# Kernel tuning notes

Measured on AMD Instinct MI355X. Metric: run time of the kernel, lower is better.

Reference implementation:

```python
import jax, jax.numpy as jnp
import numpy as np


def _conv(x, k):
    # x: (B,H,W,Cin), k: (kh,kw,Cin,Cout), SAME padding, stride 1
    return jax.lax.conv_general_dilated(
        x, k, window_strides=(1, 1), padding='SAME',
        dimension_numbers=('NHWC', 'HWIO', 'NHWC'))


def _hard_sigmoid(x):
    # Keras ConvLSTM2D default recurrent_activation='hard_sigmoid'
    return jnp.clip(0.2 * x + 0.5, 0.0, 1.0)


def _convlstm_layer(x_seq, k, rk, b):
    # x_seq: (B,T,H,W,Cin); gates packed i,f,c,o along channel axis (Keras order)
    B, T, H, W, _ = x_seq.shape
    F = rk.shape[2]
    h0 = jnp.zeros((B, H, W, F), x_seq.dtype)
    c0 = jnp.zeros((B, H, W, F), x_seq.dtype)

    def step(carry, xt):
        h, c = carry
        z = _conv(xt, k) + _conv(h, rk) + b
        i, f, g, o = jnp.split(z, 4, axis=-1)
        c_new = _hard_sigmoid(f) * c + _hard_sigmoid(i) * jnp.tanh(g)
        h_new = _hard_sigmoid(o) * jnp.tanh(c_new)
        return (h_new, c_new), h_new

    (h, c), ys = jax.lax.scan(step, (h0, c0), jnp.moveaxis(x_seq, 1, 0))
    return jnp.moveaxis(ys, 0, 1), h, c  # outputs (B,T,H,W,F), final h, c


def setup_inputs() -> dict:
    key = jax.random.key(0)
    ks = jax.random.split(key, 6)
    s = 0.05
    return {
        'x': jax.random.normal(ks[0], (8, 10, 64, 64, 1), jnp.float32),
        'k0': jax.random.normal(ks[1], (3, 3, 1, 256), jnp.float32) * s,
        'rk0': jax.random.normal(ks[2], (3, 3, 64, 256), jnp.float32) * s,
        'b0': jnp.zeros((256,), jnp.float32),
        'k1': jax.random.normal(ks[3], (3, 3, 64, 256), jnp.float32) * s,
        'rk1': jax.random.normal(ks[4], (3, 3, 64, 256), jnp.float32) * s,
        'b1': jnp.zeros((256,), jnp.float32),
    }


def reference(x, k0, rk0, b0, k1, rk1, b1):
    # layer 0
    seq0, h0, c0 = _convlstm_layer(x, k0, rk0, b0)
    # layer 1 consumes layer-0 sequence
    _, h1, c1 = _convlstm_layer(seq0, k1, rk1, b1)
    # states list [[h0,c0],[h1,c1]] -> stacked (layers=2, 2, B, H, W, F)
    return jnp.stack([jnp.stack([h0, c0]), jnp.stack([h1, c1])])
```

## Files before the change

### kernel.cpp

```cpp
#include <hip/hip_runtime.h>
#include <hip/hip_bf16.h>

typedef unsigned short u16;
typedef __attribute__((ext_vector_type(8))) short short8;
typedef __attribute__((ext_vector_type(4))) float f32x4;

#define T_STEPS 10
#define NB 8
#define HH 64
#define WW 64
#define FF 64
#define NGATE 256
#define HP 66
#define PIX (NB*HH*WW)

__device__ __forceinline__ u16 f2bf(float f) {
    unsigned u = __float_as_uint(f);
    u += 0x7FFF + ((u >> 16) & 1);
    return (u16)(u >> 16);
}
__device__ __forceinline__ float hsig(float x) {
    return fminf(fmaxf(0.2f * x + 0.5f, 0.0f), 1.0f);
}
__device__ __forceinline__ float ftanh(float x) {
    float e = __expf(2.0f * x);
    return 1.0f - 2.0f / (e + 1.0f);
}
__device__ __forceinline__ void gll16(const void* g, void* l) {
    __builtin_amdgcn_global_load_lds(
        (const __attribute__((address_space(1))) unsigned*)g,
        (__attribute__((address_space(3))) unsigned*)l, 16, 0, 0);
}

__global__ void wtrans_kernel(const float* __restrict__ W0,
                              const float* __restrict__ W1,
                              u16* __restrict__ BS, int K) {
    int total = (K >> 6) << 14;
    for (int o = blockIdx.x * blockDim.x + threadIdx.x; o < total;
         o += gridDim.x * blockDim.x) {
        int e = o & 7, lane = (o >> 3) & 63, g = (o >> 9) & 3;
        int ks = (o >> 11) & 1, fq = (o >> 12) & 3, kc = o >> 14;
        int quad = lane >> 4, l15 = lane & 15;
        int n = g * 64 + fq * 16 + l15;
        int k = kc * 64 + ks * 32 + quad * 8 + e;
        float v = (k < 576) ? W0[k * NGATE + n] : W1[(k - 576) * NGATE + n];
        BS[o] = f2bf(v);
    }
}

__global__ __launch_bounds__(256, 3)
void fused_step_kernel(const u16* __restrict__ h0_prev, u16* __restrict__ h0_new,
                       const u16* __restrict__ h1_prev, u16* __restrict__ h1_new,
                       const u16* __restrict__ B0S, const u16* __restrict__ B1S,
                       const float* __restrict__ x, const float* __restrict__ k0w,
                       const float* __restrict__ b0, const float* __restrict__ b1,
                       float* __restrict__ c0, float* __restrict__ c1,
                       float* __restrict__ oh0, float* __restrict__ oc0,
                       float* __restrict__ oh1, float* __restrict__ oc1,
                       int u) {
    int blk = blockIdx.x;
    int b = blk & 7;
    int k = blk >> 3;
    int role = ((k >> 5) & 1) ^ 1;
    int y = (k & 31) | ((k >> 6) << 5);
    int pxb = b * 64 + y;
    if (role == 0 && u >= T_STEPS) return;
    if (role == 1 && u == 0) return;

    __shared__ __align__(16) u16 sA[6 * 528 * 8];
    __shared__ float xs[3][WW + 2];

    int tid = threadIdx.x;
    int lane = tid & 63, fq = tid >> 6;
    int quad = lane >> 4, l15 = lane & 15;

    const u16* BS = role ? B1S : B0S;
    int nch = role ? 18 : 9;

    if (role == 0 && tid < 3 * (WW + 2)) {
        int dyi = tid / (WW + 2), xx = tid - dyi * (WW + 2);
        int yy = y + dyi - 1, col = xx - 1;
        float v = 0.0f;
        if (yy >= 0 && yy < HH && col >= 0 && col < WW)
            v = x[(((size_t)b * T_STEPS + u) * HH + yy) * WW + col];
        xs[dyi][xx] = v;
    }

    {
        int nst = role ? 6 * 528 : 3 * 528;
        for (int i = tid; i < nst; i += 256) {
            int srcsel = i >= 3 * 528;
            int q = srcsel ? i - 3 * 528 : i;
            int r = q / 528;
            int qr = q - r * 528;
            int p = qr >> 3;
            int cb = (qr & 7) ^ (p & 7);
            const u16* src = srcsel ? h1_prev : h0_prev;
            gll16(src + (((size_t)(b * HP + y + r)) * HP + p) * FF + cb * 8,
                  &sA[(size_t)i * 8]);
        }
    }
    asm volatile("s_waitcnt vmcnt(0) lgkmcnt(0)\n\ts_barrier" ::: "memory");

    f32x4 acc[4][4];
#pragma unroll
    for (int mt = 0; mt < 4; ++mt)
#pragma unroll
        for (int g = 0; g < 4; ++g)
            acc[mt][g] = (f32x4){0.f, 0.f, 0.f, 0.f};

    const u16* bbase = BS + (fq << 12) + lane * 8;
    short8 bA[8], bB[8];

#pragma unroll
    for (int j = 0; j < 8; ++j)
        bA[j] = *(const short8*)(bbase + ((j >> 2) << 11) + ((j & 3) << 9));

    int dx = 0, srb = 0;

#define KBODY(BC, BN, kcur)                                                   \
    {                                                                         \
        int kn = (kcur) + 1 < nch ? (kcur) + 1 : (kcur);                      \
        const u16* bpn = bbase + ((size_t)kn << 14);                          \
        _Pragma("unroll")                                                     \
        for (int j = 0; j < 8; ++j)                                           \
            BN[j] = *(const short8*)(bpn + ((j >> 2) << 11) + ((j & 3) << 9)); \
        int cc = l15 + dx, sw = cc & 7;                                       \
        const u16* ar = sA + srb + cc * 64;                                   \
        _Pragma("unroll")                                                     \
        for (int ks = 0; ks < 2; ++ks) {                                      \
            short8 aF[4];                                                     \
            int so = (((ks << 2) | quad) ^ sw) << 3;                          \
            _Pragma("unroll")                                                 \
            for (int mt = 0; mt < 4; ++mt)                                    \
                aF[mt] = *(const short8*)(ar + so + mt * 1024);               \
            _Pragma("unroll")                                                 \
            for (int mt = 0; mt < 4; ++mt)                                    \
                _Pragma("unroll")                                             \
                for (int g = 0; g < 4; ++g)                                   \
                    acc[mt][g] = __builtin_amdgcn_mfma_f32_16x16x32_bf16(     \
                        aF[mt], BC[ks * 4 + g], acc[mt][g], 0, 0, 0);         \
        }                                                                     \
        ++dx; if (dx == 3) { dx = 0; srb += 4224; }                           \
    }

    int kc = 0;
    for (; kc + 1 < nch; kc += 2) {
        KBODY(bA, bB, kc);
        KBODY(bB, bA, kc + 1);
    }
    if (kc < nch) KBODY(bA, bB, kc);
#undef KBODY

    const float* bias = role ? b1 : b0;
    float* cbuf = role ? c1 : c0;
    u16* hout = role ? h1_new : h0_new;
    int wo = role ? (u == T_STEPS) : (u == T_STEPS - 1);
    float* outh = role ? oh1 : oh0;
    float* outc = role ? oc1 : oc0;

    int f = fq * 16 + l15;
    float bi = bias[f], bff = bias[64 + f], bg = bias[128 + f], bo = bias[192 + f];
    float wk[4][9];
    if (role == 0) {
#pragma unroll
        for (int g = 0; g < 4; ++g)
#pragma unroll
            for (int tau = 0; tau < 9; ++tau)
                wk[g][tau] = k0w[tau * NGATE + g * 64 + f];
    }
#pragma unroll
    for (int mt = 0; mt < 4; ++mt) {
#pragma unroll
        for (int r = 0; r < 4; ++r) {
            int xcol = mt * 16 + quad * 4 + r;
            size_t p = (size_t)pxb * 64 + xcol;
            float zi = acc[mt][0][r] + bi;
            float zf = acc[mt][1][r] + bff;
            float zg = acc[mt][2][r] + bg;
            float zo = acc[mt][3][r] + bo;
            if (role == 0) {
#pragma unroll
                for (int tau = 0; tau < 9; ++tau) {
                    float xv = xs[tau / 3][xcol + tau % 3];
                    zi += xv * wk[0][tau];
                    zf += xv * wk[1][tau];
                    zg += xv * wk[2][tau];
                    zo += xv * wk[3][tau];
                }
            }
            float cold = cbuf[p * FF + f];
            float cn = hsig(zf) * cold + hsig(zi) * ftanh(zg);
            float hn = hsig(zo) * ftanh(cn);
            cbuf[p * FF + f] = cn;
            hout[(((size_t)(b * HP + y + 1)) * HP + (xcol + 1)) * FF + f] = f2bf(hn);
            if (wo) { outh[p * FF + f] = hn; outc[p * FF + f] = cn; }
        }
    }
}

extern "C" void kernel_launch(void* const* d_in, const int* in_sizes, int n_in,
                              void* d_out, int out_size, void* d_ws, size_t ws_size,
                              hipStream_t stream) {
    const float* x   = (const float*)d_in[0];
    const float* k0  = (const float*)d_in[1];
    const float* rk0 = (const float*)d_in[2];
    const float* b0  = (const float*)d_in[3];
    const float* k1  = (const float*)d_in[4];
    const float* rk1 = (const float*)d_in[5];
    const float* b1  = (const float*)d_in[6];
    float* out = (float*)d_out;

    char* ws = (char*)d_ws;
    const size_t HPAD_BYTES = (size_t)NB * HP * HP * FF * 2;
    const size_t C_BYTES    = (size_t)PIX * FF * 4;

    u16* h0p[2]; u16* h1p[2];
    h0p[0] = (u16*)(ws);
    h0p[1] = (u16*)(ws + HPAD_BYTES);
    h1p[0] = (u16*)(ws + 2 * HPAD_BYTES);
    h1p[1] = (u16*)(ws + 3 * HPAD_BYTES);
    float* c0 = (float*)(ws + 4 * HPAD_BYTES);
    float* c1 = (float*)(ws + 4 * HPAD_BYTES + C_BYTES);
    u16* B0S  = (u16*)(ws + 4 * HPAD_BYTES + 2 * C_BYTES);
    u16* B1S  = (u16*)(ws + 4 * HPAD_BYTES + 2 * C_BYTES + (size_t)9 * 16384 * 2);

    hipMemsetAsync(ws, 0, 4 * HPAD_BYTES + 2 * C_BYTES, stream);

    wtrans_kernel<<<512, 256, 0, stream>>>(rk0, rk0, B0S, 576);
    wtrans_kernel<<<512, 256, 0, stream>>>(k1, rk1, B1S, 1152);

    float* oh0 = out;
    float* oc0 = out + (size_t)PIX * FF;
    float* oh1 = out + 2 * (size_t)PIX * FF;
    float* oc1 = out + 3 * (size_t)PIX * FF;

    for (int u = 0; u <= T_STEPS; ++u) {
        const u16* h0_prev = h0p[(u + 1) & 1];
        u16*       h0_new  = h0p[u & 1];
        const u16* h1_prev = h1p[u & 1];
        u16*       h1_new  = h1p[(u + 1) & 1];
        fused_step_kernel<<<1024, 256, 0, stream>>>(
            h0_prev, h0_new, h1_prev, h1_new, B0S, B1S,
            x, k0, b0, b1, c0, c1, oh0, oc0, oh1, oc1, u);
    }
}
```

Baseline: 503.7 us.

## Merge layer-0 and layer-1 work into one block sharing staged h0 rows

Before, each time step launched 1024 blocks, split into separate layer-0 and layer-1 roles, and each role staged its own copy of the h0_prev halo rows into LDS. Now each of 512 blocks stages h0_prev (and h1_prev) once, then runs the layer-0 GEMM and epilogue followed by the layer-1 GEMM and epilogue in sequence. This removes the duplicated h0 staging and halves block-launch overhead. In exchange, per-block serial work grows and parallelism halves, which may leave the GPU underfilled given 3 blocks per CU.

```diff
diff --git a/kernel.cpp b/kernel.cpp
--- a/kernel.cpp
+++ b/kernel.cpp
@@ -48,76 +48,16 @@
     }
 }
 
-__global__ __launch_bounds__(256, 3)
-void fused_step_kernel(const u16* __restrict__ h0_prev, u16* __restrict__ h0_new,
-                       const u16* __restrict__ h1_prev, u16* __restrict__ h1_new,
-                       const u16* __restrict__ B0S, const u16* __restrict__ B1S,
-                       const float* __restrict__ x, const float* __restrict__ k0w,
-                       const float* __restrict__ b0, const float* __restrict__ b1,
-                       float* __restrict__ c0, float* __restrict__ c1,
-                       float* __restrict__ oh0, float* __restrict__ oc0,
-                       float* __restrict__ oh1, float* __restrict__ oc1,
-                       int u) {
-    int blk = blockIdx.x;
-    int b = blk & 7;
-    int k = blk >> 3;
-    int role = ((k >> 5) & 1) ^ 1;
-    int y = (k & 31) | ((k >> 6) << 5);
-    int pxb = b * 64 + y;
-    if (role == 0 && u >= T_STEPS) return;
-    if (role == 1 && u == 0) return;
-
-    __shared__ __align__(16) u16 sA[6 * 528 * 8];
-    __shared__ float xs[3][WW + 2];
-
-    int tid = threadIdx.x;
-    int lane = tid & 63, fq = tid >> 6;
-    int quad = lane >> 4, l15 = lane & 15;
-
-    const u16* BS = role ? B1S : B0S;
-    int nch = role ? 18 : 9;
-
-    if (role == 0 && tid < 3 * (WW + 2)) {
-        int dyi = tid / (WW + 2), xx = tid - dyi * (WW + 2);
-        int yy = y + dyi - 1, col = xx - 1;
-        float v = 0.0f;
-        if (yy >= 0 && yy < HH && col >= 0 && col < WW)
-            v = x[(((size_t)b * T_STEPS + u) * HH + yy) * WW + col];
-        xs[dyi][xx] = v;
-    }
-
-    {
-        int nst = role ? 6 * 528 : 3 * 528;
-        for (int i = tid; i < nst; i += 256) {
-            int srcsel = i >= 3 * 528;
-            int q = srcsel ? i - 3 * 528 : i;
-            int r = q / 528;
-            int qr = q - r * 528;
-            int p = qr >> 3;
-            int cb = (qr & 7) ^ (p & 7);
-            const u16* src = srcsel ? h1_prev : h0_prev;
-            gll16(src + (((size_t)(b * HP + y + r)) * HP + p) * FF + cb * 8,
-                  &sA[(size_t)i * 8]);
-        }
-    }
-    asm volatile("s_waitcnt vmcnt(0) lgkmcnt(0)\n\ts_barrier" ::: "memory");
-
-    f32x4 acc[4][4];
-#pragma unroll
-    for (int mt = 0; mt < 4; ++mt)
-#pragma unroll
-        for (int g = 0; g < 4; ++g)
-            acc[mt][g] = (f32x4){0.f, 0.f, 0.f, 0.f};
-
+__device__ __forceinline__ void kphase(f32x4 (&acc)[4][4],
+                                       const u16* __restrict__ BS, int nch,
+                                       const u16* __restrict__ sA,
+                                       int lane, int fq, int quad, int l15) {
     const u16* bbase = BS + (fq << 12) + lane * 8;
     short8 bA[8], bB[8];
-
 #pragma unroll
     for (int j = 0; j < 8; ++j)
         bA[j] = *(const short8*)(bbase + ((j >> 2) << 11) + ((j & 3) << 9));
-
     int dx = 0, srb = 0;
-
 #define KBODY(BC, BN, kcur)                                                   \
     {                                                                         \
         int kn = (kcur) + 1 < nch ? (kcur) + 1 : (kcur);                      \
@@ -143,7 +83,6 @@
         }                                                                     \
         ++dx; if (dx == 3) { dx = 0; srb += 4224; }                           \
     }
-
     int kc = 0;
     for (; kc + 1 < nch; kc += 2) {
         KBODY(bA, bB, kc);
@@ -151,18 +90,22 @@
     }
     if (kc < nch) KBODY(bA, bB, kc);
 #undef KBODY
-
-    const float* bias = role ? b1 : b0;
-    float* cbuf = role ? c1 : c0;
-    u16* hout = role ? h1_new : h0_new;
-    int wo = role ? (u == T_STEPS) : (u == T_STEPS - 1);
-    float* outh = role ? oh1 : oh0;
-    float* outc = role ? oc1 : oc0;
-
+}
+
+__device__ __forceinline__ void epilogue(const f32x4 (&acc)[4][4],
+                                         const float* __restrict__ bias,
+                                         float* __restrict__ cbuf,
+                                         u16* __restrict__ hout,
+                                         float* __restrict__ outh,
+                                         float* __restrict__ outc, int wo,
+                                         int withx, const float (*xs)[WW + 2],
+                                         const float* __restrict__ k0w,
+                                         int b, int y, int pxb,
+                                         int fq, int quad, int l15) {
     int f = fq * 16 + l15;
     float bi = bias[f], bff = bias[64 + f], bg = bias[128 + f], bo = bias[192 + f];
     float wk[4][9];
-    if (role == 0) {
+    if (withx) {
 #pragma unroll
         for (int g = 0; g < 4; ++g)
 #pragma unroll
@@ -179,7 +122,7 @@
             float zf = acc[mt][1][r] + bff;
             float zg = acc[mt][2][r] + bg;
             float zo = acc[mt][3][r] + bo;
-            if (role == 0) {
+            if (withx) {
 #pragma unroll
                 for (int tau = 0; tau < 9; ++tau) {
                     float xv = xs[tau / 3][xcol + tau % 3];
@@ -199,6 +142,80 @@
     }
 }
 
+__global__ __launch_bounds__(256, 3)
+void fused_step_kernel(const u16* __restrict__ h0_prev, u16* __restrict__ h0_new,
+                       const u16* __restrict__ h1_prev, u16* __restrict__ h1_new,
+                       const u16* __restrict__ B0S, const u16* __restrict__ B1S,
+                       const float* __restrict__ x, const float* __restrict__ k0w,
+                       const float* __restrict__ b0, const float* __restrict__ b1,
+                       float* __restrict__ c0, float* __restrict__ c1,
+                       float* __restrict__ oh0, float* __restrict__ oc0,
+                       float* __restrict__ oh1, float* __restrict__ oc1,
+                       int u) {
+    int blk = blockIdx.x;
+    int b = blk & 7;
+    int y = blk >> 3;
+    int pxb = b * 64 + y;
+    int do0 = (u < T_STEPS);
+    int do1 = (u > 0);
+
+    __shared__ __align__(16) u16 sA[6 * 528 * 8];
+    __shared__ float xs[3][WW + 2];
+
+    int tid = threadIdx.x;
+    int lane = tid & 63, fq = tid >> 6;
+    int quad = lane >> 4, l15 = lane & 15;
+
+    if (do0 && tid < 3 * (WW + 2)) {
+        int dyi = tid / (WW + 2), xx = tid - dyi * (WW + 2);
+        int yy = y + dyi - 1, col = xx - 1;
+        float v = 0.0f;
+        if (yy >= 0 && yy < HH && col >= 0 && col < WW)
+            v = x[(((size_t)b * T_STEPS + u) * HH + yy) * WW + col];
+        xs[dyi][xx] = v;
+    }
+
+    {
+        int nst = do1 ? 6 * 528 : 3 * 528;
+        for (int i = tid; i < nst; i += 256) {
+            int srcsel = i >= 3 * 528;
+            int q = srcsel ? i - 3 * 528 : i;
+            int r = q / 528;
+            int qr = q - r * 528;
+            int p = qr >> 3;
+            int cb = (qr & 7) ^ (p & 7);
+            const u16* src = srcsel ? h1_prev : h0_prev;
+            gll16(src + (((size_t)(b * HP + y + r)) * HP + p) * FF + cb * 8,
+                  &sA[(size_t)i * 8]);
+        }
+    }
+    asm volatile("s_waitcnt vmcnt(0) lgkmcnt(0)\n\ts_barrier" ::: "memory");
+
+    f32x4 acc[4][4];
+
+    if (do0) {
+#pragma unroll
+        for (int mt = 0; mt < 4; ++mt)
+#pragma unroll
+            for (int g = 0; g < 4; ++g)
+                acc[mt][g] = (f32x4){0.f, 0.f, 0.f, 0.f};
+        kphase(acc, B0S, 9, sA, lane, fq, quad, l15);
+        epilogue(acc, b0, c0, h0_new, oh0, oc0, u == T_STEPS - 1,
+                 1, xs, k0w, b, y, pxb, fq, quad, l15);
+    }
+
+    if (do1) {
+#pragma unroll
+        for (int mt = 0; mt < 4; ++mt)
+#pragma unroll
+            for (int g = 0; g < 4; ++g)
+                acc[mt][g] = (f32x4){0.f, 0.f, 0.f, 0.f};
+        kphase(acc, B1S, 18, sA, lane, fq, quad, l15);
+        epilogue(acc, b1, c1, h1_new, oh1, oc1, u == T_STEPS,
+                 0, xs, k0w, b, y, pxb, fq, quad, l15);
+    }
+}
+
 extern "C" void kernel_launch(void* const* d_in, const int* in_sizes, int n_in,
                               void* d_out, int out_size, void* d_ws, size_t ws_size,
                               hipStream_t stream) {
@@ -240,7 +257,7 @@
         u16*       h0_new  = h0p[u & 1];
         const u16* h1_prev = h1p[u & 1];
         u16*       h1_new  = h1p[(u + 1) & 1];
-        fused_step_kernel<<<1024, 256, 0, stream>>>(
+        fused_step_kernel<<<512, 256, 0, stream>>>(
             h0_prev, h0_new, h1_prev, h1_new, B0S, B1S,
             x, k0, b0, b1, c0, c1, oh0, oc0, oh1, oc1, u);
     }
```

After: 504.2 us. No clear change (+0.1%).
